# Optimization experiments

Measured on AMD Instinct MI355X. Metric: run time of the kernel, lower is better.

## Reference

```python
import jax, jax.numpy as jnp
import numpy as np

B, S, D, H = 32, 512, 512, 8  # note: source requires S == D due to swapped shape tuple in multi_head_attention
DK = D // H  # 64
FF = 200     # hard-coded FFN width in source
LN_EPS = 1e-5


def setup_inputs() -> dict:
    key = jax.random.key(0)
    ks = jax.random.split(key, 20)
    s = 0.02
    return {
        "x": jax.random.normal(ks[0], (B, S, D), dtype=jnp.float32),
        # per-head projections, stacked: torch Linear weight shape is [out, in] = [DK, D]
        "Wq": jax.random.normal(ks[1], (H, DK, D), dtype=jnp.float32) * s,
        "bq": jax.random.normal(ks[2], (H, DK), dtype=jnp.float32) * s,
        "Wk": jax.random.normal(ks[3], (H, DK, D), dtype=jnp.float32) * s,
        "bk": jax.random.normal(ks[4], (H, DK), dtype=jnp.float32) * s,
        "Wv": jax.random.normal(ks[5], (H, DK, D), dtype=jnp.float32) * s,
        "bv": jax.random.normal(ks[6], (H, DK), dtype=jnp.float32) * s,
        "Wo": jax.random.normal(ks[7], (D, D), dtype=jnp.float32) * s,
        "bo": jax.random.normal(ks[8], (D,), dtype=jnp.float32) * s,
        "W1": jax.random.normal(ks[9], (FF, D), dtype=jnp.float32) * s,
        "b1": jax.random.normal(ks[10], (FF,), dtype=jnp.float32) * s,
        "W2": jax.random.normal(ks[11], (FF, FF), dtype=jnp.float32) * s,
        "b2": jax.random.normal(ks[12], (FF,), dtype=jnp.float32) * s,
        "W3": jax.random.normal(ks[13], (D, FF), dtype=jnp.float32) * s,
        "b3": jax.random.normal(ks[14], (D,), dtype=jnp.float32) * s,
        # single SHARED LayerNorm over last two dims (S, D)
        "gamma": jnp.ones((S, D), dtype=jnp.float32),
        "beta": jnp.zeros((S, D), dtype=jnp.float32),
    }


def _layernorm2d(y, gamma, beta):
    # torch LayerNorm(normalized_shape=(S, D)): normalize over last two axes, biased variance
    m = jnp.mean(y, axis=(-2, -1), keepdims=True)
    v = jnp.mean(jnp.square(y - m), axis=(-2, -1), keepdims=True)
    return (y - m) * jax.lax.rsqrt(v + LN_EPS) * gamma + beta


def reference(x, Wq, bq, Wk, bk, Wv, bv, Wo, bo, W1, b1, W2, b2, W3, b3, gamma, beta):
    # --- multi-head attention (vectorized over the original per-head Python loop) ---
    q = jnp.einsum('bsd,hkd->bhsk', x, Wq) + bq[None, :, None, :]
    k = jnp.einsum('bsd,hkd->bhsk', x, Wk) + bk[None, :, None, :]
    v = jnp.einsum('bsd,hkd->bhsk', x, Wv) + bv[None, :, None, :]
    scores = jnp.einsum('bhsk,bhtk->bhst', q, k) / jnp.sqrt(jnp.float32(DK))
    attn = jax.nn.softmax(scores, axis=-1)
    heads = jnp.einsum('bhst,bhtk->bhsk', attn, v)          # [B,H,S,DK]
    concat = heads.transpose(0, 2, 1, 3).reshape(B, S, D)    # concat heads along feature dim
    y = jnp.einsum('bsd,ed->bse', concat, Wo) + bo + x       # output proj + residual
    # --- post-attention LayerNorm (shared params) ---
    y = _layernorm2d(y, gamma, beta)
    # --- feed-forward: D -> 200 -> 200 -> D, residual, LayerNorm (same shared LN) ---
    f = jax.nn.relu(jnp.einsum('bsd,fd->bsf', y, W1) + b1)
    f = jax.nn.relu(jnp.einsum('bsf,gf->bsg', f, W2) + b2)
    f = jnp.einsum('bsf,df->bsd', f, W3) + b3
    y = _layernorm2d(f + y, gamma, beta)
    # --- final LayerNorm (same shared LN again) ---
    return _layernorm2d(y, gamma, beta)
```

## Files before the change

kernel.cpp:

```cpp
#include <hip/hip_runtime.h>
#include <hip/hip_bf16.h>
#include <stdint.h>

#define B_  32
#define S_  512
#define D_  512
#define H_  8
#define DK_ 64
#define FF_ 200
#define FFP 256
#define M_  (B_*S_)
#define MSD ((size_t)B_*S_*D_)
#define NQKV 1536

typedef __hip_bfloat16 bf16;
typedef __attribute__((ext_vector_type(8))) short short8;
typedef __attribute__((ext_vector_type(4))) float f32x4;
typedef __attribute__((ext_vector_type(4))) unsigned short us4;

__device__ inline float b2f(bf16 v) { return __bfloat162float(v); }
__device__ inline bf16  f2b(float v){ return __float2bfloat16(v); }
__device__ inline unsigned short f2bu(float v) {
  union { bf16 h; unsigned short u; } cv; cv.h = __float2bfloat16(v); return cv.u;
}
__device__ inline float bu2f(unsigned short u) {
  union { unsigned short u; bf16 h; } cv; cv.u = u; return b2f(cv.h);
}
__device__ __forceinline__ void async16(const bf16* g, bf16* l) {
  __builtin_amdgcn_global_load_lds((const __attribute__((address_space(1))) void*)g,
                                   (__attribute__((address_space(3))) void*)l, 16, 0, 0);
}

__global__ void detect_kernel(const unsigned short* __restrict__ xu, int* __restrict__ flag,
                              float* __restrict__ stats) {
  __shared__ int mx[256];
  const int tid = threadIdx.x;
  if (tid < 192) stats[tid] = 0.f;
  int m = 0;
  for (int i = tid * 2; i < 8192; i += 512) {
    int e = (xu[i] >> 7) & 0xFF;
    m = m > e ? m : e;
  }
  mx[tid] = m;
  __syncthreads();
  for (int st = 128; st; st >>= 1) {
    if (tid < st) mx[tid] = mx[tid] > mx[tid + st] ? mx[tid] : mx[tid + st];
    __syncthreads();
  }
  if (tid == 0) *flag = (mx[0] >= 0xC0) ? 1 : 0;
}

__global__ __launch_bounds__(256) void cvt_x8(const void* __restrict__ in, bf16* __restrict__ out,
                                              const int* __restrict__ flag) {
  const bool f32in = (*flag != 0);
  size_t i = ((size_t)blockIdx.x * 256 + threadIdx.x) * 8;
  const size_t stride = (size_t)gridDim.x * 256 * 8;
  for (; i < MSD; i += stride) {
    if (f32in) {
      const float4 a = ((const float4*)in)[i/4];
      const float4 b = ((const float4*)in)[i/4 + 1];
      uint4 o; unsigned short* po = (unsigned short*)&o;
      po[0]=f2bu(a.x); po[1]=f2bu(a.y); po[2]=f2bu(a.z); po[3]=f2bu(a.w);
      po[4]=f2bu(b.x); po[5]=f2bu(b.y); po[6]=f2bu(b.z); po[7]=f2bu(b.w);
      *(uint4*)((unsigned short*)out + i) = o;
    } else {
      *(uint4*)((unsigned short*)out + i) = *(const uint4*)((const unsigned short*)in + i);
    }
  }
}

struct Seg { const void* src; void* dst; int srcRows, srcK, dstK, total; };
struct Segs { Seg s[16]; unsigned int isbf; };

__global__ __launch_bounds__(256) void cvt_all(Segs sg, const int* __restrict__ flag) {
  const bool f32in = (*flag != 0);
  const int seg = blockIdx.x & 15;
  const Seg sd = sg.s[seg];
  const int stride = (gridDim.x >> 4) * 256;
  const bool nopad = (sd.srcK == sd.dstK);
  for (int i = (blockIdx.x >> 4) * 256 + threadIdx.x; i < sd.total; i += stride) {
    int sidx; bool valid;
    if (nopad) { sidx = i; valid = (i < sd.srcRows * sd.srcK); }
    else {
      int r = i / sd.dstK, c = i - r * sd.dstK;
      valid = (r < sd.srcRows) && (c < sd.srcK);
      sidx = r * sd.srcK + c;
    }
    float v = 0.f;
    if (valid) v = f32in ? ((const float*)sd.src)[sidx] : b2f(((const bf16*)sd.src)[sidx]);
    if (sg.isbf & (1u << seg)) ((unsigned short*)sd.dst)[i] = f2bu(v);
    else                       ((float*)sd.dst)[i] = v;
  }
}

template<int MODE, int STATS>
__global__ __launch_bounds__(256) void gemm_mfma(
    const bf16* __restrict__ A, const bf16* __restrict__ W, const float* __restrict__ bias,
    const bf16* __restrict__ R, bf16* __restrict__ C, int M, int N, int K,
    float* __restrict__ stats)
{
  __shared__ __align__(16) char smem[49152];
  bf16*  As  = (bf16*)smem;
  bf16*  Bs  = (bf16*)(smem + 24576);
  float* Lf  = (float*)smem;
  float* red = (float*)(smem + 16896);

  const int tid  = threadIdx.x;
  const int bm   = blockIdx.x * 128;
  const int bn   = blockIdx.y * 128;
  const int w    = tid >> 6;
  const int lane = tid & 63;
  const int qd   = lane >> 4;
  const int ln   = lane & 15;
  const int wr   = (w >> 1) * 64;
  const int wc   = (w & 1) * 64;

  const int r0 = lane >> 2;
  const int ch = (lane & 3) * 8;
  const bf16* Ag0 = A + (size_t)(bm + w*16 + r0) * K + ch;
  const bf16* Ag1 = Ag0 + (size_t)64 * K;
  const bf16* Bg0 = W + (size_t)(bn + w*16 + r0) * K + ch;
  const bf16* Bg1 = Bg0 + (size_t)64 * K;
  const int lo = w*512 + lane*8;

  f32x4 acc[4][4] = {};
  const int nt = K >> 5;

  async16(Ag0, As + lo);
  async16(Ag1, As + lo + 2048);
  async16(Bg0, Bs + lo);
  async16(Bg1, Bs + lo + 2048);
  async16(Ag0 + 32, As + 4096 + lo);
  async16(Ag1 + 32, As + 4096 + lo + 2048);
  async16(Bg0 + 32, Bs + 4096 + lo);
  async16(Bg1 + 32, Bs + 4096 + lo + 2048);

  int pcur = 0;
  for (int t = 0; t < nt; t++) {
    if (t + 1 < nt) {
      asm volatile("s_waitcnt vmcnt(4)" ::: "memory");
    } else {
      asm volatile("s_waitcnt vmcnt(0)" ::: "memory");
    }
    __builtin_amdgcn_s_barrier();

    const int cur = pcur << 12;
    short8 af[4], bfr[4];
#pragma unroll
    for (int i = 0; i < 4; i++) af[i]  = *(const short8*)(As + cur + (wr + i*16 + ln)*32 + qd*8);
#pragma unroll
    for (int j = 0; j < 4; j++) bfr[j] = *(const short8*)(Bs + cur + (wc + j*16 + ln)*32 + qd*8);

    if (t + 2 < nt) {
      int pst = pcur - 1; if (pst < 0) pst = 2;
      const int nxt = pst << 12;
      const int k0  = (t + 2) << 5;
      async16(Ag0 + k0, As + nxt + lo);
      async16(Ag1 + k0, As + nxt + lo + 2048);
      async16(Bg0 + k0, Bs + nxt + lo);
      async16(Bg1 + k0, Bs + nxt + lo + 2048);
    }

#pragma unroll
    for (int i = 0; i < 4; i++)
#pragma unroll
      for (int j = 0; j < 4; j++)
        acc[i][j] = __builtin_amdgcn_mfma_f32_16x16x32_bf16(af[i], bfr[j], acc[i][j], 0, 0, 0);

    pcur = pcur + 1 == 3 ? 0 : pcur + 1;
  }
  __syncthreads();

  float s_acc = 0.f, ss_acc = 0.f;
  const int lrbase = (w >> 1)*16 + qd*4;
#pragma unroll
  for (int i = 0; i < 4; i++) {
#pragma unroll
    for (int j = 0; j < 4; j++) {
      const int col = wc + j*16 + ln;
#pragma unroll
      for (int rg = 0; rg < 4; rg++)
        Lf[(lrbase + rg)*132 + col] = acc[i][j][rg];
    }
    __syncthreads();
#pragma unroll
    for (int pz = 0; pz < 2; pz++) {
      const int q   = tid + pz*256;
      const int r   = q >> 4;
      const int nof = (q & 15)*8;
      const int m   = bm + (r >> 4)*64 + i*16 + (r & 15);
      const int n   = bn + nof;
      f32x4 v0 = *(const f32x4*)(Lf + r*132 + nof);
      f32x4 v1 = *(const f32x4*)(Lf + r*132 + nof + 4);
      f32x4 b0 = *(const f32x4*)(bias + n);
      f32x4 b1 = *(const f32x4*)(bias + n + 4);
      float vals[8];
#pragma unroll
      for (int e = 0; e < 4; e++) { vals[e] = v0[e] + b0[e]; vals[4+e] = v1[e] + b1[e]; }
      if (MODE == 1) {
#pragma unroll
        for (int e = 0; e < 8; e++) vals[e] = fmaxf(vals[e], 0.f);
      }
      if (MODE == 2) {
        const uint4 rv = *(const uint4*)((const unsigned short*)R + (size_t)m * N + n);
        const unsigned short* rp = (const unsigned short*)&rv;
#pragma unroll
        for (int e = 0; e < 8; e++) vals[e] += bu2f(rp[e]);
      }
      if (STATS) {
#pragma unroll
        for (int e = 0; e < 8; e++) { s_acc += vals[e]; ss_acc += vals[e]*vals[e]; }
      }
      uint4 o; unsigned short* op = (unsigned short*)&o;
#pragma unroll
      for (int e = 0; e < 8; e++) op[e] = f2bu(vals[e]);
      *(uint4*)((unsigned short*)C + (size_t)m * N + n) = o;
    }
    __syncthreads();
  }

  if (STATS) {
    red[tid] = s_acc; red[256 + tid] = ss_acc;
    __syncthreads();
    for (int st = 128; st; st >>= 1) {
      if (tid < st) { red[tid] += red[tid + st]; red[256 + tid] += red[256 + tid + st]; }
      __syncthreads();
    }
    if (tid == 0) {
      const int b = bm >> 9;
      atomicAdd(&stats[b*2],     red[0]);
      atomicAdd(&stats[b*2 + 1], red[256]);
    }
  }
}

__global__ __launch_bounds__(1024, 4) void attn_lds(const bf16* __restrict__ qkv,
                                                    bf16* __restrict__ cat)
{
  __shared__ bf16 Ks[2 * 512 * 32];
  __shared__ bf16 Vs[64 * 520];
  __shared__ bf16 pbuf[16][16][40];

  const int tid  = threadIdx.x;
  const int w    = tid >> 6;
  const int lane = tid & 63;
  const int qd   = lane >> 4;
  const int ln   = lane & 15;
  const int bh   = blockIdx.x;
  const int b    = bh >> 3, h = bh & 7;
  const bf16* base = qkv + (size_t)b * 512 * NQKV + h * 64;

#pragma unroll
  for (int r = 0; r < 2; r++) {
    int c = tid + r*1024;
    int part = c & 3, key = (c >> 2) & 255, ks = c >> 10;
    async16(base + (size_t)key * NQKV + 512 + ks*32 + part*8,
            Ks + ks*16384 + key*32 + part*8);
  }
#pragma unroll
  for (int r = 0; r < 2; r++) {
    int c = tid + r*1024;
    int dkg = c >> 8, key = c & 255;
    uint4 vv = *(const uint4*)(base + (size_t)key * NQKV + 1024 + dkg*8);
    const unsigned short* pv = (const unsigned short*)&vv;
#pragma unroll
    for (int j = 0; j < 8; j++)
      *(unsigned short*)&Vs[(dkg*8 + j)*520 + key] = pv[j];
  }
  short8 bq[2][2];
#pragma unroll
  for (int qt = 0; qt < 2; qt++)
#pragma unroll
    for (int ks = 0; ks < 2; ks++)
      bq[qt][ks] = *(const short8*)(base + (size_t)(w*32 + qt*16 + ln) * NQKV + ks*32 + qd*8);

  __syncthreads();

#pragma unroll
  for (int r = 0; r < 2; r++) {
    int c = tid + r*1024;
    int part = c & 3, key = 256 + ((c >> 2) & 255), ks = c >> 10;
    async16(base + (size_t)key * NQKV + 512 + ks*32 + part*8,
            Ks + ks*16384 + key*32 + part*8);
  }
  uint4 vhold[2]; int vdst[2];
#pragma unroll
  for (int r = 0; r < 2; r++) {
    int c = tid + r*1024;
    int dkg = c >> 8, key = 256 + (c & 255);
    vhold[r] = *(const uint4*)(base + (size_t)key * NQKV + 1024 + dkg*8);
    vdst[r] = dkg*8*520 + key;
  }
  asm volatile("" ::: "memory");

  bf16 (*pb)[40] = pbuf[w];
  f32x4 o[2][4] = {};
  float l[2] = {0.f, 0.f};

  for (int half = 0; half < 2; half++) {
    for (int st = half*8; st < half*8 + 8; st++) {
      short8 ak[2][2];
#pragma unroll
      for (int kt = 0; kt < 2; kt++)
#pragma unroll
        for (int ks = 0; ks < 2; ks++)
          ak[kt][ks] = *(const short8*)(Ks + ks*16384 + (st*32 + kt*16 + ln)*32 + qd*8);
      f32x4 s[2][2] = {};
#pragma unroll
      for (int kt = 0; kt < 2; kt++)
#pragma unroll
        for (int qt = 0; qt < 2; qt++) {
          s[kt][qt] = __builtin_amdgcn_mfma_f32_16x16x32_bf16(ak[kt][0], bq[qt][0], s[kt][qt], 0, 0, 0);
          s[kt][qt] = __builtin_amdgcn_mfma_f32_16x16x32_bf16(ak[kt][1], bq[qt][1], s[kt][qt], 0, 0, 0);
        }
      float e[2][2][4];
#pragma unroll
      for (int kt = 0; kt < 2; kt++)
#pragma unroll
        for (int qt = 0; qt < 2; qt++)
#pragma unroll
          for (int rg = 0; rg < 4; rg++) {
            float ev = __expf(s[kt][qt][rg] * 0.125f);
            e[kt][qt][rg] = ev;
            l[qt] += ev;
          }
#pragma unroll
      for (int qt = 0; qt < 2; qt++) {
#pragma unroll
        for (int kt = 0; kt < 2; kt++) {
          uint2 pk;
          pk.x = (unsigned)f2bu(e[kt][qt][0]) | ((unsigned)f2bu(e[kt][qt][1]) << 16);
          pk.y = (unsigned)f2bu(e[kt][qt][2]) | ((unsigned)f2bu(e[kt][qt][3]) << 16);
          *(uint2*)&pb[ln][kt*16 + qd*4] = pk;
        }
        short8 ap = *(const short8*)&pb[ln][qd*8];
#pragma unroll
        for (int nt = 0; nt < 4; nt++) {
          short8 bv = *(const short8*)(Vs + (nt*16 + ln)*520 + st*32 + qd*8);
          o[qt][nt] = __builtin_amdgcn_mfma_f32_16x16x32_bf16(ap, bv, o[qt][nt], 0, 0, 0);
        }
      }
    }
    if (half == 0) {
      asm volatile("s_waitcnt vmcnt(0)" ::: "memory");
#pragma unroll
      for (int r = 0; r < 2; r++) {
        const unsigned short* pv = (const unsigned short*)&vhold[r];
#pragma unroll
        for (int j = 0; j < 8; j++)
          *(unsigned short*)&Vs[vdst[r] + j*520] = pv[j];
      }
      asm volatile("s_waitcnt lgkmcnt(0)" ::: "memory");
      __builtin_amdgcn_s_barrier();
    }
  }

#pragma unroll
  for (int qt = 0; qt < 2; qt++) {
    l[qt] += __shfl_xor(l[qt], 16);
    l[qt] += __shfl_xor(l[qt], 32);
  }
  float inv0 = 1.f / l[0], inv1 = 1.f / l[1];

  const size_t crow0 = (size_t)(b*S_ + w*32) * D_ + h*DK_;
#pragma unroll
  for (int qt = 0; qt < 2; qt++) {
#pragma unroll
    for (int rg = 0; rg < 4; rg++) {
      float ivv = __shfl(qt ? inv1 : inv0, qd*4 + rg);
      int r = qt*16 + qd*4 + rg;
      bf16* cp = cat + crow0 + (size_t)r * D_ + ln;
#pragma unroll
      for (int nt = 0; nt < 4; nt++) cp[nt*16] = f2b(o[qt][nt][rg] * ivv);
    }
  }
}

__global__ __launch_bounds__(256) void ln_b16_b16(const bf16* __restrict__ in,
    const float* __restrict__ stats, const bf16* __restrict__ gamma,
    const bf16* __restrict__ beta, bf16* __restrict__ out)
{
  const int b = blockIdx.x >> 4;
  const float invN = 1.f / (float)(S_*D_);
  const float m    = stats[b*2] * invN;
  const float var  = stats[b*2+1] * invN - m*m;
  const float rstd = rsqrtf(var + 1e-5f);
  size_t v = (size_t)b * 65536 + (blockIdx.x & 15) * 4096 + threadIdx.x;
#pragma unroll 4
  for (int it = 0; it < 16; it++, v += 256) {
    us4 xi = *(const us4*)((const unsigned short*)in + v*4);
    size_t e = (v * 4) & (S_*D_ - 1);
    us4 g4 = *(const us4*)((const unsigned short*)gamma + e);
    us4 b4 = *(const us4*)((const unsigned short*)beta + e);
    us4 o;
    o[0] = f2bu((bu2f(xi[0]) - m) * rstd * bu2f(g4[0]) + bu2f(b4[0]));
    o[1] = f2bu((bu2f(xi[1]) - m) * rstd * bu2f(g4[1]) + bu2f(b4[1]));
    o[2] = f2bu((bu2f(xi[2]) - m) * rstd * bu2f(g4[2]) + bu2f(b4[2]));
    o[3] = f2bu((bu2f(xi[3]) - m) * rstd * bu2f(g4[3]) + bu2f(b4[3]));
    *(us4*)((unsigned short*)out + v*4) = o;
  }
}

__global__ __launch_bounds__(256) void ln_b16_b16_stats(const bf16* __restrict__ in,
    const float* __restrict__ stats, const bf16* __restrict__ gamma,
    const bf16* __restrict__ beta, bf16* __restrict__ out, float* __restrict__ stats3)
{
  __shared__ float red[512];
  const int b = blockIdx.x >> 4;
  const float invN = 1.f / (float)(S_*D_);
  const float m    = stats[b*2] * invN;
  const float var  = stats[b*2+1] * invN - m*m;
  const float rstd = rsqrtf(var + 1e-5f);
  size_t v = (size_t)b * 65536 + (blockIdx.x & 15) * 4096 + threadIdx.x;
  float s_acc = 0.f, ss_acc = 0.f;
#pragma unroll 4
  for (int it = 0; it < 16; it++, v += 256) {
    us4 xi = *(const us4*)((const unsigned short*)in + v*4);
    size_t e = (v * 4) & (S_*D_ - 1);
    us4 g4 = *(const us4*)((const unsigned short*)gamma + e);
    us4 b4 = *(const us4*)((const unsigned short*)beta + e);
    float o0 = (bu2f(xi[0]) - m) * rstd * bu2f(g4[0]) + bu2f(b4[0]);
    float o1 = (bu2f(xi[1]) - m) * rstd * bu2f(g4[1]) + bu2f(b4[1]);
    float o2 = (bu2f(xi[2]) - m) * rstd * bu2f(g4[2]) + bu2f(b4[2]);
    float o3 = (bu2f(xi[3]) - m) * rstd * bu2f(g4[3]) + bu2f(b4[3]);
    us4 o;
    o[0] = f2bu(o0); o[1] = f2bu(o1); o[2] = f2bu(o2); o[3] = f2bu(o3);
    s_acc  += o0 + o1 + o2 + o3;
    ss_acc += o0*o0 + o1*o1 + o2*o2 + o3*o3;
    *(us4*)((unsigned short*)out + v*4) = o;
  }
  const int tid = threadIdx.x;
  red[tid] = s_acc; red[256 + tid] = ss_acc;
  __syncthreads();
  for (int st = 128; st; st >>= 1) {
    if (tid < st) { red[tid] += red[tid + st]; red[256 + tid] += red[256 + tid + st]; }
    __syncthreads();
  }
  if (tid == 0) {
    atomicAdd(&stats3[b*2],     red[0]);
    atomicAdd(&stats3[b*2 + 1], red[256]);
  }
}

__global__ __launch_bounds__(256) void ln_apply_out(const bf16* __restrict__ in,
    const float* __restrict__ stats, const bf16* __restrict__ gamma,
    const bf16* __restrict__ beta, void* __restrict__ out, const int* __restrict__ flag)
{
  const bool f32 = (*flag != 0);
  const int b = blockIdx.x >> 4;
  const float invN = 1.f / (float)(S_*D_);
  const float m    = stats[b*2] * invN;
  const float var  = stats[b*2+1] * invN - m*m;
  const float rstd = rsqrtf(var + 1e-5f);
  size_t v = (size_t)b * 65536 + (blockIdx.x & 15) * 4096 + threadIdx.x;
#pragma unroll 4
  for (int it = 0; it < 16; it++, v += 256) {
    us4 xi = *(const us4*)((const unsigned short*)in + v*4);
    size_t e = (v * 4) & (S_*D_ - 1);
    us4 g4 = *(const us4*)((const unsigned short*)gamma + e);
    us4 b4 = *(const us4*)((const unsigned short*)beta + e);
    float4 o;
    o.x = (bu2f(xi[0]) - m) * rstd * bu2f(g4[0]) + bu2f(b4[0]);
    o.y = (bu2f(xi[1]) - m) * rstd * bu2f(g4[1]) + bu2f(b4[1]);
    o.z = (bu2f(xi[2]) - m) * rstd * bu2f(g4[2]) + bu2f(b4[2]);
    o.w = (bu2f(xi[3]) - m) * rstd * bu2f(g4[3]) + bu2f(b4[3]);
    if (f32) ((float4*)out)[v] = o;
    else {
      us4 ob;
      ob[0] = f2bu(o.x); ob[1] = f2bu(o.y); ob[2] = f2bu(o.z); ob[3] = f2bu(o.w);
      *(us4*)((unsigned short*)out + v*4) = ob;
    }
  }
}

extern "C" void kernel_launch(void* const* d_in, const int* in_sizes, int n_in,
                              void* d_out, int out_size, void* d_ws, size_t ws_size,
                              hipStream_t stream)
{
  char* p = (char*)d_ws;
  auto alloc_b = [&](size_t elems) { void* r = p; p += elems * 2; return (bf16*)r; };
  auto alloc_f = [&](size_t elems) {
    p = (char*)(((uintptr_t)p + 15) & ~(uintptr_t)15); void* r = p; p += elems * 4; return (float*)r;
  };

  bf16* xb   = alloc_b(MSD);
  bf16* qkv  = alloc_b(3 * MSD);
  bf16* catb = alloc_b(MSD);
  bf16* wqkv = alloc_b(3 * 512 * 512);
  bf16* wo   = alloc_b(512 * 512);
  bf16* w1p  = alloc_b((size_t)FFP * 512);
  bf16* w2p  = alloc_b((size_t)FFP * FFP);
  bf16* w3p  = alloc_b((size_t)512 * FFP);
  bf16* gm   = alloc_b((size_t)S_ * D_);
  bf16* bt   = alloc_b((size_t)S_ * D_);
  float* bqkv= alloc_f(3 * 512);
  float* bo  = alloc_f(512);
  float* b1p = alloc_f(FFP);
  float* b2p = alloc_f(FFP);
  float* b3  = alloc_f(512);
  float* stats = alloc_f(192);
  int*   flag  = (int*)alloc_f(16);
  if ((size_t)(p - (char*)d_ws) > ws_size) return;

  bf16* y1b = qkv;
  bf16* f1  = qkv + MSD;
  bf16* f2  = qkv + MSD + (size_t)M_ * FFP;
  bf16* yA  = qkv + 2 * MSD;
  bf16* yB  = catb;
  bf16* y2b = yA;
  float* st1 = stats, *st2 = stats + 64, *st3 = stats + 128;

  detect_kernel<<<1, 256, 0, stream>>>((const unsigned short*)d_in[0], flag, stats);
  cvt_x8<<<2048, 256, 0, stream>>>(d_in[0], xb, flag);

  Segs sg;
  sg.s[0]  = { d_in[1],  wqkv,               512, 512, 512, 512*512 };
  sg.s[1]  = { d_in[3],  wqkv + 512*512,     512, 512, 512, 512*512 };
  sg.s[2]  = { d_in[5],  wqkv + 2*512*512,   512, 512, 512, 512*512 };
  sg.s[3]  = { d_in[7],  wo,                 512, 512, 512, 512*512 };
  sg.s[4]  = { d_in[9],  w1p,                FF_, 512, 512, FFP*512 };
  sg.s[5]  = { d_in[11], w2p,                FF_, FF_, FFP, FFP*FFP };
  sg.s[6]  = { d_in[13], w3p,                512, FF_, FFP, 512*FFP };
  sg.s[7]  = { d_in[2],  bqkv,               1, 512, 512, 512 };
  sg.s[8]  = { d_in[4],  bqkv + 512,         1, 512, 512, 512 };
  sg.s[9]  = { d_in[6],  bqkv + 1024,        1, 512, 512, 512 };
  sg.s[10] = { d_in[8],  bo,                 1, 512, 512, 512 };
  sg.s[11] = { d_in[10], b1p,                1, FF_, FFP, FFP };
  sg.s[12] = { d_in[12], b2p,                1, FF_, FFP, FFP };
  sg.s[13] = { d_in[14], b3,                 1, 512, 512, 512 };
  sg.s[14] = { d_in[15], gm,                 1, S_*D_, S_*D_, S_*D_ };
  sg.s[15] = { d_in[16], bt,                 1, S_*D_, S_*D_, S_*D_ };
  sg.isbf = 0xC07F;
  cvt_all<<<1024, 256, 0, stream>>>(sg, flag);

  dim3 blk(256);

  gemm_mfma<0, 0><<<dim3(M_/128, NQKV/128), blk, 0, stream>>>(
      xb, wqkv, bqkv, nullptr, qkv, M_, NQKV, 512, nullptr);

  attn_lds<<<B_*H_, 1024, 0, stream>>>(qkv, catb);

  gemm_mfma<2, 1><<<dim3(M_/128, 4), blk, 0, stream>>>(
      catb, wo, bo, xb, yA, M_, 512, 512, st1);

  ln_b16_b16<<<512, blk, 0, stream>>>(yA, st1, gm, bt, y1b);

  gemm_mfma<1, 0><<<dim3(M_/128, 2), blk, 0, stream>>>(
      y1b, w1p, b1p, nullptr, f1, M_, FFP, 512, nullptr);
  gemm_mfma<1, 0><<<dim3(M_/128, 2), blk, 0, stream>>>(
      f1, w2p, b2p, nullptr, f2, M_, FFP, FFP, nullptr);
  gemm_mfma<2, 1><<<dim3(M_/128, 4), blk, 0, stream>>>(
      f2, w3p, b3, y1b, yB, M_, 512, FFP, st2);

  ln_b16_b16_stats<<<512, blk, 0, stream>>>(yB, st2, gm, bt, y2b, st3);
  ln_apply_out<<<512, blk, 0, stream>>>(y2b, st3, gm, bt, d_out, flag);
}
```

Before: 276.4 us.

## Fuse last two LayerNorms by deriving second LN stats algebraically

The second LayerNorm's mean and variance are now computed in closed form from extra moment sums (sums weighted by gamma, gamma squared and gamma times beta) gathered in the W3 GEMM epilogue, plus constant gamma/beta moments from a small new kernel. This removes one full read-write pass over the activation tensor and one kernel launch. The GEMM epilogue now also loads gamma and beta and accumulates six reductions instead of two. The expanded-moment variance formula in fp32 risks cancellation error.

```diff
diff --git a/kernel.cpp b/kernel.cpp
--- a/kernel.cpp
+++ b/kernel.cpp
@@ -35,7 +35,7 @@
                               float* __restrict__ stats) {
   __shared__ int mx[256];
   const int tid = threadIdx.x;
-  if (tid < 192) stats[tid] = 0.f;
+  if (tid < 160) { stats[tid] = 0.f; stats[tid + 160] = 0.f; }
   int m = 0;
   for (int i = tid * 2; i < 8192; i += 512) {
     int e = (xu[i] >> 7) & 0xFF;
@@ -93,11 +93,40 @@
   }
 }
 
+__global__ __launch_bounds__(256) void gb_stats(const bf16* __restrict__ g,
+    const bf16* __restrict__ b, float* __restrict__ cst) {
+  __shared__ float red[5][256];
+  const int tid = threadIdx.x;
+  float c0=0.f, c1=0.f, c2=0.f, c3=0.f, c4=0.f;
+#pragma unroll
+  for (int k = 0; k < 4; k++) {
+    const int grp = blockIdx.x*256 + tid + k*16384;
+    us4 g4 = *(const us4*)((const unsigned short*)g + grp*4);
+    us4 b4 = *(const us4*)((const unsigned short*)b + grp*4);
+#pragma unroll
+    for (int j = 0; j < 4; j++) {
+      float G = bu2f(g4[j]), B = bu2f(b4[j]);
+      c0 += G; c1 += G*G; c2 += G*B; c3 += B; c4 += B*B;
+    }
+  }
+  red[0][tid]=c0; red[1][tid]=c1; red[2][tid]=c2; red[3][tid]=c3; red[4][tid]=c4;
+  __syncthreads();
+  for (int st = 128; st; st >>= 1) {
+    if (tid < st)
+#pragma unroll
+      for (int q = 0; q < 5; q++) red[q][tid] += red[q][tid + st];
+    __syncthreads();
+  }
+  if (tid == 0)
+#pragma unroll
+    for (int q = 0; q < 5; q++) atomicAdd(&cst[q], red[q][0]);
+}
+
 template<int MODE, int STATS>
 __global__ __launch_bounds__(256) void gemm_mfma(
     const bf16* __restrict__ A, const bf16* __restrict__ W, const float* __restrict__ bias,
     const bf16* __restrict__ R, bf16* __restrict__ C, int M, int N, int K,
-    float* __restrict__ stats)
+    float* __restrict__ stats, const bf16* __restrict__ gmp, const bf16* __restrict__ btp)
 {
   __shared__ __align__(16) char smem[49152];
   bf16*  As  = (bf16*)smem;
@@ -172,6 +201,7 @@
   __syncthreads();
 
   float s_acc = 0.f, ss_acc = 0.f;
+  float a2 = 0.f, a3 = 0.f, a4 = 0.f, a5 = 0.f;
   const int lrbase = (w >> 1)*16 + qd*4;
 #pragma unroll
   for (int i = 0; i < 4; i++) {
@@ -207,10 +237,25 @@
 #pragma unroll
         for (int e = 0; e < 8; e++) vals[e] += bu2f(rp[e]);
       }
-      if (STATS) {
+      if (STATS == 1) {
 #pragma unroll
         for (int e = 0; e < 8; e++) { s_acc += vals[e]; ss_acc += vals[e]*vals[e]; }
       }
+      if (STATS == 2) {
+        const int ei = ((m & 511) << 9) + n;
+        const uint4 gv = *(const uint4*)((const unsigned short*)gmp + ei);
+        const uint4 bv = *(const uint4*)((const unsigned short*)btp + ei);
+        const unsigned short* gp = (const unsigned short*)&gv;
+        const unsigned short* bp = (const unsigned short*)&bv;
+#pragma unroll
+        for (int e = 0; e < 8; e++) {
+          const float vv = vals[e];
+          const float G  = bu2f(gp[e]);
+          const float Bv = bu2f(bp[e]);
+          s_acc += vv; ss_acc += vv*vv;
+          a2 += G*vv; a3 += G*G*vv; a4 += G*G*vv*vv; a5 += G*Bv*vv;
+        }
+      }
       uint4 o; unsigned short* op = (unsigned short*)&o;
 #pragma unroll
       for (int e = 0; e < 8; e++) op[e] = f2bu(vals[e]);
@@ -219,7 +264,7 @@
     __syncthreads();
   }
 
-  if (STATS) {
+  if (STATS == 1) {
     red[tid] = s_acc; red[256 + tid] = ss_acc;
     __syncthreads();
     for (int st = 128; st; st >>= 1) {
@@ -230,6 +275,23 @@
       const int b = bm >> 9;
       atomicAdd(&stats[b*2],     red[0]);
       atomicAdd(&stats[b*2 + 1], red[256]);
+    }
+  }
+  if (STATS == 2) {
+    float v6[6] = { s_acc, ss_acc, a2, a3, a4, a5 };
+#pragma unroll
+    for (int q2 = 0; q2 < 6; q2++) red[q2*256 + tid] = v6[q2];
+    __syncthreads();
+    for (int st = 128; st; st >>= 1) {
+      if (tid < st)
+#pragma unroll
+        for (int q2 = 0; q2 < 6; q2++) red[q2*256 + tid] += red[q2*256 + tid + st];
+      __syncthreads();
+    }
+    if (tid == 0) {
+      const int b = bm >> 9;
+#pragma unroll
+      for (int q2 = 0; q2 < 6; q2++) atomicAdd(&stats[b*6 + q2], red[q2*256]);
     }
   }
 }
@@ -401,57 +463,26 @@
   }
 }
 
-__global__ __launch_bounds__(256) void ln_b16_b16_stats(const bf16* __restrict__ in,
-    const float* __restrict__ stats, const bf16* __restrict__ gamma,
-    const bf16* __restrict__ beta, bf16* __restrict__ out, float* __restrict__ stats3)
-{
-  __shared__ float red[512];
-  const int b = blockIdx.x >> 4;
-  const float invN = 1.f / (float)(S_*D_);
-  const float m    = stats[b*2] * invN;
-  const float var  = stats[b*2+1] * invN - m*m;
-  const float rstd = rsqrtf(var + 1e-5f);
-  size_t v = (size_t)b * 65536 + (blockIdx.x & 15) * 4096 + threadIdx.x;
-  float s_acc = 0.f, ss_acc = 0.f;
-#pragma unroll 4
-  for (int it = 0; it < 16; it++, v += 256) {
-    us4 xi = *(const us4*)((const unsigned short*)in + v*4);
-    size_t e = (v * 4) & (S_*D_ - 1);
-    us4 g4 = *(const us4*)((const unsigned short*)gamma + e);
-    us4 b4 = *(const us4*)((const unsigned short*)beta + e);
-    float o0 = (bu2f(xi[0]) - m) * rstd * bu2f(g4[0]) + bu2f(b4[0]);
-    float o1 = (bu2f(xi[1]) - m) * rstd * bu2f(g4[1]) + bu2f(b4[1]);
-    float o2 = (bu2f(xi[2]) - m) * rstd * bu2f(g4[2]) + bu2f(b4[2]);
-    float o3 = (bu2f(xi[3]) - m) * rstd * bu2f(g4[3]) + bu2f(b4[3]);
-    us4 o;
-    o[0] = f2bu(o0); o[1] = f2bu(o1); o[2] = f2bu(o2); o[3] = f2bu(o3);
-    s_acc  += o0 + o1 + o2 + o3;
-    ss_acc += o0*o0 + o1*o1 + o2*o2 + o3*o3;
-    *(us4*)((unsigned short*)out + v*4) = o;
-  }
-  const int tid = threadIdx.x;
-  red[tid] = s_acc; red[256 + tid] = ss_acc;
-  __syncthreads();
-  for (int st = 128; st; st >>= 1) {
-    if (tid < st) { red[tid] += red[tid + st]; red[256 + tid] += red[256 + tid + st]; }
-    __syncthreads();
-  }
-  if (tid == 0) {
-    atomicAdd(&stats3[b*2],     red[0]);
-    atomicAdd(&stats3[b*2 + 1], red[256]);
-  }
-}
-
-__global__ __launch_bounds__(256) void ln_apply_out(const bf16* __restrict__ in,
-    const float* __restrict__ stats, const bf16* __restrict__ gamma,
-    const bf16* __restrict__ beta, void* __restrict__ out, const int* __restrict__ flag)
+__global__ __launch_bounds__(256) void ln23_fused(const bf16* __restrict__ in,
+    const float* __restrict__ st2x, const float* __restrict__ cst,
+    const bf16* __restrict__ gamma, const bf16* __restrict__ beta,
+    void* __restrict__ out, const int* __restrict__ flag)
 {
   const bool f32 = (*flag != 0);
   const int b = blockIdx.x >> 4;
   const float invN = 1.f / (float)(S_*D_);
-  const float m    = stats[b*2] * invN;
-  const float var  = stats[b*2+1] * invN - m*m;
-  const float rstd = rsqrtf(var + 1e-5f);
+  const float Sv   = st2x[b*6+0], Svv  = st2x[b*6+1];
+  const float SGv  = st2x[b*6+2], SG2v = st2x[b*6+3];
+  const float SG2v2= st2x[b*6+4], SGBv = st2x[b*6+5];
+  const float CG = cst[0], CG2 = cst[1], CGB = cst[2], CB = cst[3], CB2 = cst[4];
+  const float m2 = Sv * invN;
+  const float r2 = rsqrtf(Svv * invN - m2*m2 + 1e-5f);
+  const float Sy  = r2 * (SGv - m2*CG) + CB;
+  const float SSy = r2*r2 * (SG2v2 - 2.f*m2*SG2v + m2*m2*CG2)
+                  + 2.f*r2 * (SGBv - m2*CGB) + CB2;
+  const float m3 = Sy * invN;
+  const float r3 = rsqrtf(SSy * invN - m3*m3 + 1e-5f);
+
   size_t v = (size_t)b * 65536 + (blockIdx.x & 15) * 4096 + threadIdx.x;
 #pragma unroll 4
   for (int it = 0; it < 16; it++, v += 256) {
@@ -460,10 +491,26 @@
     us4 g4 = *(const us4*)((const unsigned short*)gamma + e);
     us4 b4 = *(const us4*)((const unsigned short*)beta + e);
     float4 o;
-    o.x = (bu2f(xi[0]) - m) * rstd * bu2f(g4[0]) + bu2f(b4[0]);
-    o.y = (bu2f(xi[1]) - m) * rstd * bu2f(g4[1]) + bu2f(b4[1]);
-    o.z = (bu2f(xi[2]) - m) * rstd * bu2f(g4[2]) + bu2f(b4[2]);
-    o.w = (bu2f(xi[3]) - m) * rstd * bu2f(g4[3]) + bu2f(b4[3]);
+    {
+      float G = bu2f(g4[0]), B = bu2f(b4[0]);
+      float y2 = (bu2f(xi[0]) - m2) * r2 * G + B;
+      o.x = (y2 - m3) * r3 * G + B;
+    }
+    {
+      float G = bu2f(g4[1]), B = bu2f(b4[1]);
+      float y2 = (bu2f(xi[1]) - m2) * r2 * G + B;
+      o.y = (y2 - m3) * r3 * G + B;
+    }
+    {
+      float G = bu2f(g4[2]), B = bu2f(b4[2]);
+      float y2 = (bu2f(xi[2]) - m2) * r2 * G + B;
+      o.z = (y2 - m3) * r3 * G + B;
+    }
+    {
+      float G = bu2f(g4[3]), B = bu2f(b4[3]);
+      float y2 = (bu2f(xi[3]) - m2) * r2 * G + B;
+      o.w = (y2 - m3) * r3 * G + B;
+    }
     if (f32) ((float4*)out)[v] = o;
     else {
       us4 ob;
@@ -498,7 +545,7 @@
   float* b1p = alloc_f(FFP);
   float* b2p = alloc_f(FFP);
   float* b3  = alloc_f(512);
-  float* stats = alloc_f(192);
+  float* stats = alloc_f(320);
   int*   flag  = (int*)alloc_f(16);
   if ((size_t)(p - (char*)d_ws) > ws_size) return;
 
@@ -507,8 +554,9 @@
   bf16* f2  = qkv + MSD + (size_t)M_ * FFP;
   bf16* yA  = qkv + 2 * MSD;
   bf16* yB  = catb;
-  bf16* y2b = yA;
-  float* st1 = stats, *st2 = stats + 64, *st3 = stats + 128;
+  float* st1  = stats;
+  float* cst  = stats + 64;
+  float* st2x = stats + 80;
 
   detect_kernel<<<1, 256, 0, stream>>>((const unsigned short*)d_in[0], flag, stats);
   cvt_x8<<<2048, 256, 0, stream>>>(d_in[0], xb, flag);
@@ -533,25 +581,26 @@
   sg.isbf = 0xC07F;
   cvt_all<<<1024, 256, 0, stream>>>(sg, flag);
 
+  gb_stats<<<64, 256, 0, stream>>>(gm, bt, cst);
+
   dim3 blk(256);
 
   gemm_mfma<0, 0><<<dim3(M_/128, NQKV/128), blk, 0, stream>>>(
-      xb, wqkv, bqkv, nullptr, qkv, M_, NQKV, 512, nullptr);
+      xb, wqkv, bqkv, nullptr, qkv, M_, NQKV, 512, nullptr, nullptr, nullptr);
 
   attn_lds<<<B_*H_, 1024, 0, stream>>>(qkv, catb);
 
   gemm_mfma<2, 1><<<dim3(M_/128, 4), blk, 0, stream>>>(
-      catb, wo, bo, xb, yA, M_, 512, 512, st1);
+      catb, wo, bo, xb, yA, M_, 512, 512, st1, nullptr, nullptr);
 
   ln_b16_b16<<<512, blk, 0, stream>>>(yA, st1, gm, bt, y1b);
 
   gemm_mfma<1, 0><<<dim3(M_/128, 2), blk, 0, stream>>>(
-      y1b, w1p, b1p, nullptr, f1, M_, FFP, 512, nullptr);
+      y1b, w1p, b1p, nullptr, f1, M_, FFP, 512, nullptr, nullptr, nullptr);
   gemm_mfma<1, 0><<<dim3(M_/128, 2), blk, 0, stream>>>(
-      f1, w2p, b2p, nullptr, f2, M_, FFP, FFP, nullptr);
-  gemm_mfma<2, 1><<<dim3(M_/128, 4), blk, 0, stream>>>(
-      f2, w3p, b3, y1b, yB, M_, 512, FFP, st2);
-
-  ln_b16_b16_stats<<<512, blk, 0, stream>>>(yB, st2, gm, bt, y2b, st3);
-  ln_apply_out<<<512, blk, 0, stream>>>(y2b, st3, gm, bt, d_out, flag);
-}
+      f1, w2p, b2p, nullptr, f2, M_, FFP, FFP, nullptr, nullptr, nullptr);
+  gemm_mfma<2, 2><<<dim3(M_/128, 4), blk, 0, stream>>>(
+      f2, w3p, b3, y1b, yB, M_, 512, FFP, st2x, gm, bt);
+
+  ln23_fused<<<512, blk, 0, stream>>>(yB, st2x, cst, gm, bt, d_out, flag);
+}
```

Result: no change. 273.2 us (-1.2%).
